# Optimization experiments

Hardware: AMD Instinct MI355X
Metric: run time of the kernel (lower is better)

The kernel has to match this reference:

```python
import jax, jax.numpy as jnp
import numpy as np

B, T, C, HS = 32, 2048, 1024, 64

def setup_inputs() -> dict:
    key = jax.random.key(0)
    k1, k2, k3, k4 = jax.random.split(key, 4)
    x = jax.random.normal(k1, (B, T, C), dtype=jnp.float32)
    Wk = jax.random.normal(k2, (C, HS), dtype=jnp.float32) * (C ** -0.5)
    Wq = jax.random.normal(k3, (C, HS), dtype=jnp.float32) * (C ** -0.5)
    Wv = jax.random.normal(k4, (C, HS), dtype=jnp.float32) * (C ** -0.5)
    return {"x": x, "Wk": Wk, "Wq": Wq, "Wv": Wv}

def reference(x, Wk, Wq, Wv):
    # x: [B,T,C]; bias-free projections
    k = jnp.einsum('btc,ch->bth', x, Wk)   # [B,T,HS]
    q = jnp.einsum('btc,ch->bth', x, Wq)   # [B,T,HS]
    v = jnp.einsum('btc,ch->bth', x, Wv)   # [B,T,HS]
    Tdim = x.shape[1]
    Cdim = x.shape[2]
    scale = jax.lax.rsqrt(jnp.float32(Cdim))  # NOTE: source scales by rsqrt(C), not head_size
    wei = jnp.einsum('bth,bsh->bts', q, k) * scale  # [B,T,T]
    causal = jnp.tril(jnp.ones((Tdim, Tdim), dtype=bool))
    wei = jnp.where(causal, wei, -jnp.inf)
    wei = jax.nn.softmax(wei, axis=-1)
    out = jnp.einsum('bts,bsh->bth', wei, v)  # [B,T,HS]
    return out
```

## Files before the change

### kernel.cpp

```cpp
#include <hip/hip_runtime.h>
#include <hip/hip_bf16.h>

#define Bn 32
#define Tn 2048
#define Cn 1024
#define HSn 64

typedef __attribute__((ext_vector_type(8))) short short8;
typedef __attribute__((ext_vector_type(4))) float floatx4;

#if __has_builtin(__builtin_amdgcn_exp2f)
#define EXP2F __builtin_amdgcn_exp2f
#else
#define EXP2F exp2f
#endif

static __device__ __forceinline__ short f2bf(float f) {
    union { float f; unsigned u; } v; v.f = f;
    unsigned r = v.u + 0x7FFFu + ((v.u >> 16) & 1u);
    return (short)(r >> 16);
}
static __device__ __forceinline__ short f2bf_fast(float f) {
    union { float f; unsigned u; } v; v.f = f;
    return (short)((v.u + 0x8000u) >> 16);
}

static __device__ __forceinline__ void async16(const void* g, void* l) {
    __builtin_amdgcn_global_load_lds((const __attribute__((address_space(1))) void*)g,
                                     (__attribute__((address_space(3))) void*)l,
                                     16, 0, 0);
}

__global__ __launch_bounds__(256) void swz_w(const float* __restrict__ Wk,
                                             const float* __restrict__ Wq,
                                             const float* __restrict__ Wv,
                                             short* __restrict__ wswz) {
    int e = blockIdx.x * 256 + threadIdx.x;
    int j    = e & 7;
    int lane = (e >> 3) & 63;
    int grp  = e >> 9;
    int nt   = grp % 12;
    int kc   = grp / 12;
    int q = lane >> 4, m = lane & 15;
    int k = kc * 32 + q * 8 + j;
    int n = nt * 16 + m;
    const float* W = (n < 64) ? Wq : ((n < 128) ? Wk : Wv);
    wswz[e] = f2bf(W[k * 64 + (n & 63)]);
}

__global__ __launch_bounds__(256, 2) void qkv_gemm(const float* __restrict__ x,
                                                   const short* __restrict__ wswz,
                                                   short* __restrict__ qb,
                                                   short* __restrict__ kb,
                                                   short* __restrict__ vt) {
    __shared__ __align__(16) char lds[2][28 * 1024];

    int tid = threadIdx.x;
    int w = tid >> 6, l = tid & 63;
    int quad = l >> 4, m = l & 15;
    int r0 = blockIdx.x * 128;

    floatx4 acc[2][12];
#pragma unroll
    for (int r = 0; r < 2; r++)
#pragma unroll
        for (int nt = 0; nt < 12; nt++) acc[r][nt] = (floatx4)(0.0f);

    auto stage = [&](int kc, int bsel) {
        char* ab = &lds[bsel][0];
        char* bb = &lds[bsel][16 * 1024];
        int srow = l & 15, sc = l >> 4;
#pragma unroll
        for (int i = 0; i < 2; i++) {
            int rt = 2 * w + i;
            const float* rbase = x + (size_t)(r0 + rt * 16 + srow) * Cn + kc * 32;
#pragma unroll
            for (int h = 0; h < 2; h++)
                async16(rbase + h * 16 + sc * 4,
                        ab + rt * 2048 + h * 1024 + l * 16);
        }
#pragma unroll
        for (int i = 0; i < 3; i++) {
            int nt = 3 * w + i;
            const short* src = wswz + ((size_t)(kc * 12 + nt) * 64 + l) * 8;
            async16(src, bb + nt * 1024 + l * 16);
        }
    };

    int c0 = (quad & 1) * 2, hh = quad >> 1;

    stage(0, 0);
    for (int kc = 0; kc < 32; kc++) {
        __syncthreads();
        if (kc < 31) stage(kc + 1, (kc + 1) & 1);

        const char* ab = &lds[kc & 1][0];
        const char* bb = &lds[kc & 1][16 * 1024];

        short8 af[2];
#pragma unroll
        for (int r = 0; r < 2; r++) {
            int rt = 2 * w + r;
            const char* ap = ab + rt * 2048 + hh * 1024 + (c0 * 16 + m) * 16;
            float4 a0 = *(const float4*)(ap);
            float4 a1 = *(const float4*)(ap + 256);
            short8 t;
            t[0] = f2bf(a0.x); t[1] = f2bf(a0.y); t[2] = f2bf(a0.z); t[3] = f2bf(a0.w);
            t[4] = f2bf(a1.x); t[5] = f2bf(a1.y); t[6] = f2bf(a1.z); t[7] = f2bf(a1.w);
            af[r] = t;
        }
#pragma unroll
        for (int nt = 0; nt < 12; nt++) {
            short8 bf = *(const short8*)(bb + nt * 1024 + l * 16);
            acc[0][nt] = __builtin_amdgcn_mfma_f32_16x16x32_bf16(af[0], bf, acc[0][nt], 0, 0, 0);
            acc[1][nt] = __builtin_amdgcn_mfma_f32_16x16x32_bf16(af[1], bf, acc[1][nt], 0, 0, 0);
        }
    }

#pragma unroll
    for (int r = 0; r < 2; r++) {
        int rt = 2 * w + r;
#pragma unroll
        for (int reg = 0; reg < 4; reg++) {
            int g = r0 + rt * 16 + quad * 4 + reg;
            int b = g >> 11, t = g & (Tn - 1);
#pragma unroll
            for (int nt = 0; nt < 4; nt++)
                qb[(size_t)g * HSn + nt * 16 + m] = f2bf(acc[r][nt][reg]);
#pragma unroll
            for (int nt = 0; nt < 4; nt++)
                kb[(size_t)g * HSn + nt * 16 + m] = f2bf(acc[r][4 + nt][reg]);
#pragma unroll
            for (int nt = 0; nt < 4; nt++)
                vt[((size_t)b * HSn + nt * 16 + m) * Tn + t] = f2bf(acc[r][8 + nt][reg]);
        }
    }
}

__global__ __launch_bounds__(256, 2) void attn(const short* __restrict__ qb,
                                               const short* __restrict__ kb,
                                               const short* __restrict__ vt,
                                               float* __restrict__ out) {
    __shared__ __align__(16) short kbuf[2][64 * 64];
    __shared__ __align__(16) short vbuf[2][64 * 64];
    __shared__ __align__(16) short p_lds[4][16][72];

    int tid = threadIdx.x;
    int w = tid >> 6, l = tid & 63;
    int quad = l >> 4, m = l & 15;
    int b = blockIdx.x >> 4;
    int p = blockIdx.x & 15;

    const short* kbbase = kb + (size_t)b * Tn * HSn;
    const short* vtbase = vt + (size_t)b * HSn * Tn;
    const float sl2e = 0.045084220027780106f;

    int srow8 = l >> 3;
    int schunk = l & 7;
    auto stageKV = [&](int j, int s) {
#pragma unroll
        for (int i = 0; i < 2; i++) {
            int r = w * 16 + i * 8 + srow8;
            int c = schunk ^ (r & 7);
            async16(kbbase + ((size_t)(j * 64 + r)) * HSn + c * 8,
                    (char*)&kbuf[s][(w * 16 + i * 8) * 64] + l * 16);
            async16(vtbase + (size_t)r * Tn + j * 64 + c * 8,
                    (char*)&vbuf[s][(w * 16 + i * 8) * 64] + l * 16);
        }
    };

    for (int phase = 0; phase < 2; phase++) {
        int qt = phase ? (31 - p) : p;
        int r0 = qt * 64 + w * 16;

        size_t qoff = ((size_t)b * Tn + r0 + m) * HSn;
        short8 qf0 = *(const short8*)(qb + qoff + quad * 8);
        short8 qf1 = *(const short8*)(qb + qoff + 32 + quad * 8);

        floatx4 o[4];
#pragma unroll
        for (int i = 0; i < 4; i++) o[i] = (floatx4)(0.0f);
        float ps[4] = {0.f, 0.f, 0.f, 0.f};

        stageKV(0, 0);
        for (int j = 0; j <= qt; j++) {
            __syncthreads();
            if (j < qt) stageKV(j + 1, (j + 1) & 1);

            const short* kt = &kbuf[j & 1][0];
            const short* vv = &vbuf[j & 1][0];
            int swz = m & 7;

            floatx4 s[4];
#pragma unroll
            for (int i = 0; i < 4; i++) s[i] = (floatx4)(0.0f);
#pragma unroll
            for (int kc = 0; kc < 2; kc++) {
                short8 aq = kc ? qf1 : qf0;
#pragma unroll
                for (int nt = 0; nt < 4; nt++) {
                    short8 bk = *(const short8*)(kt + (nt * 16 + m) * 64 +
                                                 ((kc * 4 + quad) ^ swz) * 8);
                    s[nt] = __builtin_amdgcn_mfma_f32_16x16x32_bf16(aq, bk, s[nt], 0, 0, 0);
                }
            }

            if (j == qt) {
                int rloc = w * 16 + quad * 4;
#pragma unroll
                for (int nt = 0; nt < 4; nt++)
#pragma unroll
                    for (int reg = 0; reg < 4; reg++) {
                        float pv = EXP2F(s[nt][reg] * sl2e);
                        pv = (nt * 16 + m > rloc + reg) ? 0.0f : pv;
                        s[nt][reg] = pv;
                        ps[reg] += pv;
                    }
            } else {
#pragma unroll
                for (int nt = 0; nt < 4; nt++)
#pragma unroll
                    for (int reg = 0; reg < 4; reg++) {
                        float pv = EXP2F(s[nt][reg] * sl2e);
                        s[nt][reg] = pv;
                        ps[reg] += pv;
                    }
            }

            asm volatile("" ::: "memory");
#pragma unroll
            for (int nt = 0; nt < 4; nt++)
#pragma unroll
                for (int reg = 0; reg < 4; reg++)
                    p_lds[w][quad * 4 + reg][nt * 16 + m] = f2bf_fast(s[nt][reg]);
            asm volatile("" ::: "memory");
            short8 ap0 = *(const short8*)(&p_lds[w][m][quad * 8]);
            short8 ap1 = *(const short8*)(&p_lds[w][m][32 + quad * 8]);

#pragma unroll
            for (int nt = 0; nt < 4; nt++) {
                short8 bv0 = *(const short8*)(vv + (nt * 16 + m) * 64 + ((0 + quad) ^ swz) * 8);
                o[nt] = __builtin_amdgcn_mfma_f32_16x16x32_bf16(ap0, bv0, o[nt], 0, 0, 0);
            }
#pragma unroll
            for (int nt = 0; nt < 4; nt++) {
                short8 bv1 = *(const short8*)(vv + (nt * 16 + m) * 64 + ((4 + quad) ^ swz) * 8);
                o[nt] = __builtin_amdgcn_mfma_f32_16x16x32_bf16(ap1, bv1, o[nt], 0, 0, 0);
            }
        }
        __syncthreads();

#pragma unroll
        for (int off = 1; off < 16; off <<= 1)
#pragma unroll
            for (int reg = 0; reg < 4; reg++)
                ps[reg] += __shfl_xor(ps[reg], off, 64);
#pragma unroll
        for (int reg = 0; reg < 4; reg++) {
            float inv = 1.0f / ps[reg];
            int g = r0 + quad * 4 + reg;
#pragma unroll
            for (int nt = 0; nt < 4; nt++)
                out[((size_t)b * Tn + g) * HSn + nt * 16 + m] = o[nt][reg] * inv;
        }
    }
}

extern "C" void kernel_launch(void* const* d_in, const int* in_sizes, int n_in,
                              void* d_out, int out_size, void* d_ws, size_t ws_size,
                              hipStream_t stream) {
    const float* x  = (const float*)d_in[0];
    const float* Wk = (const float*)d_in[1];
    const float* Wq = (const float*)d_in[2];
    const float* Wv = (const float*)d_in[3];
    float* out = (float*)d_out;

    char* ws = (char*)d_ws;
    short* wswz = (short*)ws;
    short* qb   = (short*)(ws + (1 << 19));
    short* kb   = (short*)(ws + (1 << 19) + (8 << 20));
    short* vt   = (short*)(ws + (1 << 19) + (16 << 20));

    swz_w<<<dim3(768), dim3(256), 0, stream>>>(Wk, Wq, Wv, wswz);
    qkv_gemm<<<dim3(512), dim3(256), 0, stream>>>(x, wswz, qb, kb, vt);
    attn<<<dim3(512), dim3(256), 0, stream>>>(qb, kb, vt, out);
}
```

Measured before the change: 447.2 us.

## Split attention into one block per query tile, transpose S, pack bf16 conversions

The attention kernel now launches one block per (batch, query tile) with a balanced causal tile ordering, instead of pairing two tiles per block. It also raises the occupancy hint to 4 blocks per CU. QK^T is computed transposed so each lane holds one query row, which lets the row sum stay in one register, and P is written to a swizzled LDS buffer using packed v_cvt_pk_bf16_f32. s_setprio is raised around the MFMA sections, and the projection GEMM also uses packed bf16 conversion. The risks are higher register pressure under the tighter launch bound and more block scheduling overhead.

```diff
diff --git a/kernel.cpp b/kernel.cpp
--- a/kernel.cpp
+++ b/kernel.cpp
@@ -20,9 +20,11 @@
     unsigned r = v.u + 0x7FFFu + ((v.u >> 16) & 1u);
     return (short)(r >> 16);
 }
-static __device__ __forceinline__ short f2bf_fast(float f) {
-    union { float f; unsigned u; } v; v.f = f;
-    return (short)((v.u + 0x8000u) >> 16);
+
+static __device__ __forceinline__ unsigned cvt_pk_bf16(float lo, float hi) {
+    unsigned u;
+    asm("v_cvt_pk_bf16_f32 %0, %1, %2" : "=v"(u) : "v"(lo), "v"(hi));
+    return u;
 }
 
 static __device__ __forceinline__ void async16(const void* g, void* l) {
@@ -104,10 +106,12 @@
             const char* ap = ab + rt * 2048 + hh * 1024 + (c0 * 16 + m) * 16;
             float4 a0 = *(const float4*)(ap);
             float4 a1 = *(const float4*)(ap + 256);
-            short8 t;
-            t[0] = f2bf(a0.x); t[1] = f2bf(a0.y); t[2] = f2bf(a0.z); t[3] = f2bf(a0.w);
-            t[4] = f2bf(a1.x); t[5] = f2bf(a1.y); t[6] = f2bf(a1.z); t[7] = f2bf(a1.w);
-            af[r] = t;
+            union { unsigned u[4]; short8 s; } cc;
+            cc.u[0] = cvt_pk_bf16(a0.x, a0.y);
+            cc.u[1] = cvt_pk_bf16(a0.z, a0.w);
+            cc.u[2] = cvt_pk_bf16(a1.x, a1.y);
+            cc.u[3] = cvt_pk_bf16(a1.z, a1.w);
+            af[r] = cc.s;
         }
 #pragma unroll
         for (int nt = 0; nt < 12; nt++) {
@@ -137,19 +141,23 @@
     }
 }
 
-__global__ __launch_bounds__(256, 2) void attn(const short* __restrict__ qb,
+__global__ __launch_bounds__(256, 4) void attn(const short* __restrict__ qb,
                                                const short* __restrict__ kb,
                                                const short* __restrict__ vt,
                                                float* __restrict__ out) {
     __shared__ __align__(16) short kbuf[2][64 * 64];
     __shared__ __align__(16) short vbuf[2][64 * 64];
-    __shared__ __align__(16) short p_lds[4][16][72];
+    __shared__ __align__(16) unsigned pbuf[4][16][32];
 
     int tid = threadIdx.x;
     int w = tid >> 6, l = tid & 63;
     int quad = l >> 4, m = l & 15;
-    int b = blockIdx.x >> 4;
-    int p = blockIdx.x & 15;
+
+    int bid = blockIdx.x;
+    int b = bid & 31;
+    int rank = bid >> 5;
+    int a = rank >> 3, d = rank & 7;
+    int qt = (a & 1) ? (16 * (a >> 1) + 15 - d) : (16 * (a >> 1) + d);
 
     const short* kbbase = kb + (size_t)b * Tn * HSn;
     const short* vtbase = vt + (size_t)b * HSn * Tn;
@@ -169,100 +177,104 @@
         }
     };
 
-    for (int phase = 0; phase < 2; phase++) {
-        int qt = phase ? (31 - p) : p;
-        int r0 = qt * 64 + w * 16;
-
-        size_t qoff = ((size_t)b * Tn + r0 + m) * HSn;
-        short8 qf0 = *(const short8*)(qb + qoff + quad * 8);
-        short8 qf1 = *(const short8*)(qb + qoff + 32 + quad * 8);
-
-        floatx4 o[4];
-#pragma unroll
-        for (int i = 0; i < 4; i++) o[i] = (floatx4)(0.0f);
-        float ps[4] = {0.f, 0.f, 0.f, 0.f};
-
-        stageKV(0, 0);
-        for (int j = 0; j <= qt; j++) {
-            __syncthreads();
-            if (j < qt) stageKV(j + 1, (j + 1) & 1);
-
-            const short* kt = &kbuf[j & 1][0];
-            const short* vv = &vbuf[j & 1][0];
-            int swz = m & 7;
-
-            floatx4 s[4];
-#pragma unroll
-            for (int i = 0; i < 4; i++) s[i] = (floatx4)(0.0f);
-#pragma unroll
-            for (int kc = 0; kc < 2; kc++) {
-                short8 aq = kc ? qf1 : qf0;
-#pragma unroll
-                for (int nt = 0; nt < 4; nt++) {
-                    short8 bk = *(const short8*)(kt + (nt * 16 + m) * 64 +
-                                                 ((kc * 4 + quad) ^ swz) * 8);
-                    s[nt] = __builtin_amdgcn_mfma_f32_16x16x32_bf16(aq, bk, s[nt], 0, 0, 0);
+    int r0 = qt * 64 + w * 16;
+    int qloc = w * 16 + m;
+
+    size_t qoff = ((size_t)b * Tn + r0 + m) * HSn;
+    short8 qf0 = *(const short8*)(qb + qoff + quad * 8);
+    short8 qf1 = *(const short8*)(qb + qoff + 32 + quad * 8);
+
+    floatx4 o[4];
+#pragma unroll
+    for (int i = 0; i < 4; i++) o[i] = (floatx4)(0.0f);
+    float ps = 0.0f;
+
+    int swz = m & 7;
+
+    stageKV(0, 0);
+    for (int j = 0; j <= qt; j++) {
+        __syncthreads();
+        if (j < qt) stageKV(j + 1, (j + 1) & 1);
+
+        const short* kt = &kbuf[j & 1][0];
+        const short* vv = &vbuf[j & 1][0];
+
+        floatx4 s[4];
+#pragma unroll
+        for (int i = 0; i < 4; i++) s[i] = (floatx4)(0.0f);
+        __builtin_amdgcn_s_setprio(1);
+#pragma unroll
+        for (int kc = 0; kc < 2; kc++) {
+            short8 aq = kc ? qf1 : qf0;
+#pragma unroll
+            for (int nt = 0; nt < 4; nt++) {
+                short8 bk = *(const short8*)(kt + (nt * 16 + m) * 64 +
+                                             ((kc * 4 + quad) ^ swz) * 8);
+                s[nt] = __builtin_amdgcn_mfma_f32_16x16x32_bf16(bk, aq, s[nt], 0, 0, 0);
+            }
+        }
+        __builtin_amdgcn_s_setprio(0);
+
+        if (j == qt) {
+#pragma unroll
+            for (int nt = 0; nt < 4; nt++)
+#pragma unroll
+                for (int reg = 0; reg < 4; reg++) {
+                    float pv = EXP2F(s[nt][reg] * sl2e);
+                    pv = (nt * 16 + quad * 4 + reg > qloc) ? 0.0f : pv;
+                    s[nt][reg] = pv;
+                    ps += pv;
                 }
+        } else {
+#pragma unroll
+            for (int nt = 0; nt < 4; nt++)
+#pragma unroll
+                for (int reg = 0; reg < 4; reg++) {
+                    float pv = EXP2F(s[nt][reg] * sl2e);
+                    s[nt][reg] = pv;
+                    ps += pv;
+                }
+        }
+
+        asm volatile("" ::: "memory");
+#pragma unroll
+        for (int nt = 0; nt < 4; nt++)
+#pragma unroll
+            for (int h = 0; h < 2; h++) {
+                unsigned u = cvt_pk_bf16(s[nt][2 * h], s[nt][2 * h + 1]);
+                pbuf[w][m][(((2 * nt + (quad >> 1)) ^ swz) << 2) +
+                           2 * (quad & 1) + h] = u;
             }
-
-            if (j == qt) {
-                int rloc = w * 16 + quad * 4;
-#pragma unroll
-                for (int nt = 0; nt < 4; nt++)
-#pragma unroll
-                    for (int reg = 0; reg < 4; reg++) {
-                        float pv = EXP2F(s[nt][reg] * sl2e);
-                        pv = (nt * 16 + m > rloc + reg) ? 0.0f : pv;
-                        s[nt][reg] = pv;
-                        ps[reg] += pv;
-                    }
-            } else {
-#pragma unroll
-                for (int nt = 0; nt < 4; nt++)
-#pragma unroll
-                    for (int reg = 0; reg < 4; reg++) {
-                        float pv = EXP2F(s[nt][reg] * sl2e);
-                        s[nt][reg] = pv;
-                        ps[reg] += pv;
-                    }
-            }
-
-            asm volatile("" ::: "memory");
-#pragma unroll
-            for (int nt = 0; nt < 4; nt++)
-#pragma unroll
-                for (int reg = 0; reg < 4; reg++)
-                    p_lds[w][quad * 4 + reg][nt * 16 + m] = f2bf_fast(s[nt][reg]);
-            asm volatile("" ::: "memory");
-            short8 ap0 = *(const short8*)(&p_lds[w][m][quad * 8]);
-            short8 ap1 = *(const short8*)(&p_lds[w][m][32 + quad * 8]);
-
-#pragma unroll
-            for (int nt = 0; nt < 4; nt++) {
-                short8 bv0 = *(const short8*)(vv + (nt * 16 + m) * 64 + ((0 + quad) ^ swz) * 8);
-                o[nt] = __builtin_amdgcn_mfma_f32_16x16x32_bf16(ap0, bv0, o[nt], 0, 0, 0);
-            }
-#pragma unroll
-            for (int nt = 0; nt < 4; nt++) {
-                short8 bv1 = *(const short8*)(vv + (nt * 16 + m) * 64 + ((4 + quad) ^ swz) * 8);
-                o[nt] = __builtin_amdgcn_mfma_f32_16x16x32_bf16(ap1, bv1, o[nt], 0, 0, 0);
-            }
-        }
-        __syncthreads();
-
-#pragma unroll
-        for (int off = 1; off < 16; off <<= 1)
-#pragma unroll
-            for (int reg = 0; reg < 4; reg++)
-                ps[reg] += __shfl_xor(ps[reg], off, 64);
-#pragma unroll
-        for (int reg = 0; reg < 4; reg++) {
-            float inv = 1.0f / ps[reg];
-            int g = r0 + quad * 4 + reg;
-#pragma unroll
-            for (int nt = 0; nt < 4; nt++)
-                out[((size_t)b * Tn + g) * HSn + nt * 16 + m] = o[nt][reg] * inv;
-        }
+        asm volatile("" ::: "memory");
+        const unsigned* prow = &pbuf[w][m][0];
+        short8 ap0 = *(const short8*)(prow + ((quad ^ swz) << 2));
+        short8 ap1 = *(const short8*)(prow + (((4 + quad) ^ swz) << 2));
+        asm volatile("" ::: "memory");
+
+        __builtin_amdgcn_s_setprio(1);
+#pragma unroll
+        for (int nt = 0; nt < 4; nt++) {
+            short8 bv0 = *(const short8*)(vv + (nt * 16 + m) * 64 + ((0 + quad) ^ swz) * 8);
+            o[nt] = __builtin_amdgcn_mfma_f32_16x16x32_bf16(ap0, bv0, o[nt], 0, 0, 0);
+        }
+#pragma unroll
+        for (int nt = 0; nt < 4; nt++) {
+            short8 bv1 = *(const short8*)(vv + (nt * 16 + m) * 64 + ((4 + quad) ^ swz) * 8);
+            o[nt] = __builtin_amdgcn_mfma_f32_16x16x32_bf16(ap1, bv1, o[nt], 0, 0, 0);
+        }
+        __builtin_amdgcn_s_setprio(0);
+    }
+
+    ps += __shfl_xor(ps, 16, 64);
+    ps += __shfl_xor(ps, 32, 64);
+#pragma unroll
+    for (int reg = 0; reg < 4; reg++) {
+        float den = __shfl(ps, quad * 4 + reg, 64);
+        float inv = 1.0f / den;
+        int g = r0 + quad * 4 + reg;
+#pragma unroll
+        for (int nt = 0; nt < 4; nt++)
+            out[((size_t)b * Tn + g) * HSn + nt * 16 + m] = o[nt][reg] * inv;
     }
 }
 
@@ -283,5 +295,5 @@
 
     swz_w<<<dim3(768), dim3(256), 0, stream>>>(Wk, Wq, Wv, wswz);
     qkv_gemm<<<dim3(512), dim3(256), 0, stream>>>(x, wswz, qb, kb, vt);
-    attn<<<dim3(512), dim3(256), 0, stream>>>(qb, kb, vt, out);
-}
+    attn<<<dim3(1024), dim3(256), 0, stream>>>(qb, kb, vt, out);
+}
```

After: 443.4 us. Within noise of the previous version (-0.9%).
